# Performance work log

Hardware: AMD Instinct MI355X
Metric: run time of the kernel (lower is better)

## Reference

```python
import jax, jax.numpy as jnp
import numpy as np

B, T, I, H = 64, 2048, 64, 256


def setup_inputs() -> dict:
    key = jax.random.key(0)
    ks = jax.random.split(key, 7)
    s_ih = 1.0 / np.sqrt(H)
    return {
        "x": jax.random.normal(ks[0], (B, T, I), dtype=jnp.float32),
        "W_ih": jax.random.normal(ks[1], (H, I), dtype=jnp.float32) * s_ih,
        "W_hh": jax.random.normal(ks[2], (H, H), dtype=jnp.float32) * s_ih,
        "b_ih": jax.random.normal(ks[3], (H,), dtype=jnp.float32) * s_ih,
        "b_hh": jax.random.normal(ks[4], (H,), dtype=jnp.float32) * s_ih,
        "W_fc": jax.random.normal(ks[5], (1, H), dtype=jnp.float32) * s_ih,
        "b_fc": jax.random.normal(ks[6], (1,), dtype=jnp.float32) * s_ih,
    }


def reference(x, W_ih, W_hh, b_ih, b_hh, W_fc, b_fc):
    # Precompute input projection for all timesteps: [B,T,H]
    pre = jnp.einsum('bti,hi->bth', x, W_ih) + b_ih + b_hh
    pre_t = jnp.swapaxes(pre, 0, 1)  # [T,B,H]

    def step(h, p_t):
        h_new = jnp.tanh(p_t + h @ W_hh.T)
        return h_new, h_new

    h0 = jnp.zeros((x.shape[0], W_hh.shape[0]), dtype=x.dtype)
    _, hs = jax.lax.scan(step, h0, pre_t)  # hs: [T,B,H]
    out = jnp.swapaxes(hs, 0, 1)  # [B,T,H]
    return out @ W_fc.T + b_fc  # [B,T,1]
```

## Files before the change

### kernel.cpp

```cpp
#include <hip/hip_runtime.h>

#define BB 64
#define TT 2048
#define II 64
#define HH 256

typedef __fp16 h2_t __attribute__((ext_vector_type(2)));
typedef __fp16 h8_t __attribute__((ext_vector_type(8)));

#define H2(i) __builtin_bit_cast(h2_t, (i))
#define I32(h) __builtin_bit_cast(int, (h))

#if __has_builtin(__builtin_amdgcn_fdot2)
#define FDOT2(a, b, c) __builtin_amdgcn_fdot2((a), (b), (c), false)
#else
__device__ __forceinline__ float FDOT2(h2_t a, h2_t b, float c) {
    return fmaf((float)a[0], (float)b[0], fmaf((float)a[1], (float)b[1], c));
}
#endif

__device__ __forceinline__ float ftanh(float x) {
    float e = __expf(2.0f * x);
    return 1.0f - 2.0f * __builtin_amdgcn_rcpf(e + 1.0f);
}

template <int CTRL>
__device__ __forceinline__ float dpp_add(float v) {
    int s = __builtin_amdgcn_update_dpp(0, __float_as_int(v), CTRL, 0xF, 0xF, true);
    return v + __int_as_float(s);
}
template <int CTRL>
__device__ __forceinline__ float dpp_get(float v) {
    int s = __builtin_amdgcn_update_dpp(0, __float_as_int(v), CTRL, 0xF, 0xF, true);
    return __int_as_float(s);
}
template <int PAT>
__device__ __forceinline__ float swz_get(float v) {
    return __int_as_float(__builtin_amdgcn_ds_swizzle(__float_as_int(v), PAT));
}
template <int PAT>
__device__ __forceinline__ float swz_add(float v) { return v + swz_get<PAT>(v); }

__device__ __forceinline__ float mrg4(float a, float b, int lane) {
    float t = (lane & 4) ? b : a;
    float u = (lane & 4) ? a : b;
    return t + swz_get<0x101F>(u);
}
__device__ __forceinline__ float mrg2(float a, float b, int lane) {
    float t = (lane & 2) ? b : a;
    float u = (lane & 2) ? a : b;
    return t + dpp_get<0x4E>(u);
}
__device__ __forceinline__ float mrg1(float a, float b, int lane) {
    float t = (lane & 1) ? b : a;
    float u = (lane & 1) ? a : b;
    return t + dpp_get<0xB1>(u);
}

__launch_bounds__(256, 1)
__global__ void rnn_fused(const float* __restrict__ x,
                          const float* __restrict__ W_ih,
                          const float* __restrict__ W_hh,
                          const float* __restrict__ b_ih,
                          const float* __restrict__ b_hh,
                          const float* __restrict__ W_fc,
                          const float* __restrict__ b_fc,
                          float* __restrict__ out) {
    __shared__ __align__(16) __fp16 hbuf[2][320];
    __shared__ float part[TT][8];

    const int tid  = threadIdx.x;
    const int b    = blockIdx.x;
    const int lane = tid & 63;
    const int w    = tid >> 6;
    const int o    = lane >> 3;
    const int q    = lane & 7;

    int whh_i[8][16];
    int wih_i[8][4];
#pragma unroll
    for (int r = 0; r < 8; ++r) {
        const int t_r = w * 64 + o * 8 + r;
        const float4* wr = (const float4*)(W_hh + t_r * HH + q * 32);
#pragma unroll
        for (int jv = 0; jv < 8; ++jv) {
            const float4 wv = wr[jv];
            whh_i[r][jv * 2 + 0] = I32(__builtin_amdgcn_cvt_pkrtz(wv.x, wv.y));
            whh_i[r][jv * 2 + 1] = I32(__builtin_amdgcn_cvt_pkrtz(wv.z, wv.w));
        }
        const float4* wi = (const float4*)(W_ih + t_r * II + q * 8);
        const float4 wa = wi[0], wb = wi[1];
        wih_i[r][0] = I32(__builtin_amdgcn_cvt_pkrtz(wa.x, wa.y));
        wih_i[r][1] = I32(__builtin_amdgcn_cvt_pkrtz(wa.z, wa.w));
        wih_i[r][2] = I32(__builtin_amdgcn_cvt_pkrtz(wb.x, wb.y));
        wih_i[r][3] = I32(__builtin_amdgcn_cvt_pkrtz(wb.z, wb.w));
    }
#pragma unroll
    for (int j = 0; j < 128; ++j) asm volatile("" : "+v"(((int*)whh_i)[j]));
#pragma unroll
    for (int j = 0; j < 32; ++j) asm volatile("" : "+v"(((int*)wih_i)[j]));

    const int myrow = w * 64 + lane;
    const float bias = b_ih[myrow] + b_hh[myrow];
    const float wfc  = W_fc[myrow];
    const float bfc  = b_fc[0];

    for (int idx = tid; idx < 2 * 320; idx += 256) ((__fp16*)hbuf)[idx] = (__fp16)0.0f;
    __syncthreads();

    const float* xbase = x + (size_t)b * TT * II + q * 8;
    float* outb = out + (size_t)b * TT;

    const int hoff = (w * 2 + (lane >> 5)) * 80 + (lane & 31) * 2;
    __fp16* hw0 = (__fp16*)((char*)&hbuf[0][0] + hoff);
    __fp16* hw1 = (__fp16*)((char*)&hbuf[1][0] + hoff);

    h2_t xc[4];
    {
        const float4* xp = (const float4*)(xbase);
        const float4 a = xp[0], c = xp[1];
        xc[0] = __builtin_amdgcn_cvt_pkrtz(a.x, a.y);
        xc[1] = __builtin_amdgcn_cvt_pkrtz(a.z, a.w);
        xc[2] = __builtin_amdgcn_cvt_pkrtz(c.x, c.y);
        xc[3] = __builtin_amdgcn_cvt_pkrtz(c.z, c.w);
    }

    int p = 0;
    for (int i = 0; i < TT; ++i) {
        const int rown = (i + 1 < TT) ? (i + 1) : (TT - 1);
        const float4* xpn = (const float4*)(xbase + rown * II);
        const float4 xna = xpn[0], xnc = xpn[1];

        float a0 = 0, a1 = 0, a2 = 0, a3 = 0, a4 = 0, a5 = 0, a6 = 0, a7 = 0;
        const h8_t* hp = (const h8_t*)((const char*)&hbuf[p][0] + q * 80);
#pragma unroll
        for (int jv = 0; jv < 4; ++jv) {
            const h8_t hv = hp[jv];
#pragma unroll
            for (int e = 0; e < 4; ++e) {
                const h2_t hh2 = __builtin_shufflevector(hv, hv, 0, 1);
                const h2_t he = (e == 0) ? __builtin_shufflevector(hv, hv, 0, 1)
                              : (e == 1) ? __builtin_shufflevector(hv, hv, 2, 3)
                              : (e == 2) ? __builtin_shufflevector(hv, hv, 4, 5)
                                         : __builtin_shufflevector(hv, hv, 6, 7);
                const int j = jv * 4 + e;
                a0 = FDOT2(H2(whh_i[0][j]), he, a0);
                a1 = FDOT2(H2(whh_i[1][j]), he, a1);
                a2 = FDOT2(H2(whh_i[2][j]), he, a2);
                a3 = FDOT2(H2(whh_i[3][j]), he, a3);
                a4 = FDOT2(H2(whh_i[4][j]), he, a4);
                a5 = FDOT2(H2(whh_i[5][j]), he, a5);
                a6 = FDOT2(H2(whh_i[6][j]), he, a6);
                a7 = FDOT2(H2(whh_i[7][j]), he, a7);
                (void)hh2;
            }
        }
#pragma unroll
        for (int e = 0; e < 4; ++e) {
            a0 = FDOT2(H2(wih_i[0][e]), xc[e], a0);
            a1 = FDOT2(H2(wih_i[1][e]), xc[e], a1);
            a2 = FDOT2(H2(wih_i[2][e]), xc[e], a2);
            a3 = FDOT2(H2(wih_i[3][e]), xc[e], a3);
            a4 = FDOT2(H2(wih_i[4][e]), xc[e], a4);
            a5 = FDOT2(H2(wih_i[5][e]), xc[e], a5);
            a6 = FDOT2(H2(wih_i[6][e]), xc[e], a6);
            a7 = FDOT2(H2(wih_i[7][e]), xc[e], a7);
        }

        xc[0] = __builtin_amdgcn_cvt_pkrtz(xna.x, xna.y);
        xc[1] = __builtin_amdgcn_cvt_pkrtz(xna.z, xna.w);
        xc[2] = __builtin_amdgcn_cvt_pkrtz(xnc.x, xnc.y);
        xc[3] = __builtin_amdgcn_cvt_pkrtz(xnc.z, xnc.w);

        const float A0 = mrg4(a0, a4, lane);
        const float A1 = mrg4(a1, a5, lane);
        const float A2 = mrg4(a2, a6, lane);
        const float A3 = mrg4(a3, a7, lane);
        const float B0 = mrg2(A0, A2, lane);
        const float B1 = mrg2(A1, A3, lane);
        const float C0 = mrg1(B0, B1, lane);

        const float hn = ftanh(C0 + bias);
        const int pn = p ^ 1;
        if (pn) hw1[0] = (__fp16)hn; else hw0[0] = (__fp16)hn;

        float c = hn * wfc;
        c = dpp_add<0xB1>(c);
        c = dpp_add<0x4E>(c);
        c = swz_add<0x101F>(c);
        c = dpp_add<0x140>(c);
        c = swz_add<0x401F>(c);
        if ((lane & 31) == 0) part[i][w * 2 + (lane >> 5)] = c;

        __syncthreads();
        p = pn;
    }

    for (int i = tid; i < TT; i += 256) {
        const float4* pp = (const float4*)&part[i][0];
        const float4 s0 = pp[0], s1 = pp[1];
        outb[i] = s0.x + s0.y + s0.z + s0.w + s1.x + s1.y + s1.z + s1.w + bfc;
    }
}

extern "C" void kernel_launch(void* const* d_in, const int* in_sizes, int n_in,
                              void* d_out, int out_size, void* d_ws, size_t ws_size,
                              hipStream_t stream) {
    const float* x    = (const float*)d_in[0];
    const float* W_ih = (const float*)d_in[1];
    const float* W_hh = (const float*)d_in[2];
    const float* b_ih = (const float*)d_in[3];
    const float* b_hh = (const float*)d_in[4];
    const float* W_fc = (const float*)d_in[5];
    const float* b_fc = (const float*)d_in[6];
    float* out = (float*)d_out;

    rnn_fused<<<BB, 256, 0, stream>>>(x, W_ih, W_hh, b_ih, b_hh, W_fc, b_fc, out);
}
```

Measured before the change: 1.323 ms.

## Split recurrent rows across 512 threads with paired lanes per row

Doubles the block to 512 threads so each thread holds 4 rows of W_hh/W_ih instead of 8. This halves the per-step dot-product chain and register footprint, at the cost of one fewer merge stage and each hidden unit being computed redundantly by a lane pair. Only even lanes write h, and W_fc is halved so the duplicated output reduction sums correctly. The output partials buffer is padded to stride 17, and one swizzle in the FC reduction is replaced by a DPP row_half_mirror. The trade-off is more waves taking part in every per-step barrier.

Result: slower. 1.367 ms (+3.4%).

```diff
diff --git a/kernel.cpp b/kernel.cpp
--- a/kernel.cpp
+++ b/kernel.cpp
@@ -4,6 +4,7 @@
 #define TT 2048
 #define II 64
 #define HH 256
+#define PSTR 17
 
 typedef __fp16 h2_t __attribute__((ext_vector_type(2)));
 typedef __fp16 h8_t __attribute__((ext_vector_type(8)));
@@ -51,13 +52,8 @@
     float u = (lane & 2) ? a : b;
     return t + dpp_get<0x4E>(u);
 }
-__device__ __forceinline__ float mrg1(float a, float b, int lane) {
-    float t = (lane & 1) ? b : a;
-    float u = (lane & 1) ? a : b;
-    return t + dpp_get<0xB1>(u);
-}
-
-__launch_bounds__(256, 1)
+
+__launch_bounds__(512, 2)
 __global__ void rnn_fused(const float* __restrict__ x,
                           const float* __restrict__ W_ih,
                           const float* __restrict__ W_hh,
@@ -67,7 +63,7 @@
                           const float* __restrict__ b_fc,
                           float* __restrict__ out) {
     __shared__ __align__(16) __fp16 hbuf[2][320];
-    __shared__ float part[TT][8];
+    __shared__ float part[TT * PSTR];
 
     const int tid  = threadIdx.x;
     const int b    = blockIdx.x;
@@ -76,11 +72,11 @@
     const int o    = lane >> 3;
     const int q    = lane & 7;
 
-    int whh_i[8][16];
-    int wih_i[8][4];
-#pragma unroll
-    for (int r = 0; r < 8; ++r) {
-        const int t_r = w * 64 + o * 8 + r;
+    int whh_i[4][16];
+    int wih_i[4][4];
+#pragma unroll
+    for (int r = 0; r < 4; ++r) {
+        const int t_r = w * 32 + o * 4 + r;
         const float4* wr = (const float4*)(W_hh + t_r * HH + q * 32);
 #pragma unroll
         for (int jv = 0; jv < 8; ++jv) {
@@ -96,22 +92,22 @@
         wih_i[r][3] = I32(__builtin_amdgcn_cvt_pkrtz(wb.z, wb.w));
     }
 #pragma unroll
-    for (int j = 0; j < 128; ++j) asm volatile("" : "+v"(((int*)whh_i)[j]));
-#pragma unroll
-    for (int j = 0; j < 32; ++j) asm volatile("" : "+v"(((int*)wih_i)[j]));
-
-    const int myrow = w * 64 + lane;
+    for (int j = 0; j < 64; ++j) asm volatile("" : "+v"(((int*)whh_i)[j]));
+#pragma unroll
+    for (int j = 0; j < 16; ++j) asm volatile("" : "+v"(((int*)wih_i)[j]));
+
+    const int myrow = w * 32 + o * 4 + ((lane >> 1) & 3);
     const float bias = b_ih[myrow] + b_hh[myrow];
-    const float wfc  = W_fc[myrow];
+    const float wfc  = W_fc[myrow] * 0.5f;
     const float bfc  = b_fc[0];
 
-    for (int idx = tid; idx < 2 * 320; idx += 256) ((__fp16*)hbuf)[idx] = (__fp16)0.0f;
+    for (int idx = tid; idx < 2 * 320; idx += 512) ((__fp16*)hbuf)[idx] = (__fp16)0.0f;
     __syncthreads();
 
     const float* xbase = x + (size_t)b * TT * II + q * 8;
     float* outb = out + (size_t)b * TT;
 
-    const int hoff = (w * 2 + (lane >> 5)) * 80 + (lane & 31) * 2;
+    const int hoff = (myrow >> 5) * 80 + (myrow & 31) * 2;
     __fp16* hw0 = (__fp16*)((char*)&hbuf[0][0] + hoff);
     __fp16* hw1 = (__fp16*)((char*)&hbuf[1][0] + hoff);
 
@@ -131,14 +127,13 @@
         const float4* xpn = (const float4*)(xbase + rown * II);
         const float4 xna = xpn[0], xnc = xpn[1];
 
-        float a0 = 0, a1 = 0, a2 = 0, a3 = 0, a4 = 0, a5 = 0, a6 = 0, a7 = 0;
+        float a0 = 0, a1 = 0, a2 = 0, a3 = 0;
         const h8_t* hp = (const h8_t*)((const char*)&hbuf[p][0] + q * 80);
 #pragma unroll
         for (int jv = 0; jv < 4; ++jv) {
             const h8_t hv = hp[jv];
 #pragma unroll
             for (int e = 0; e < 4; ++e) {
-                const h2_t hh2 = __builtin_shufflevector(hv, hv, 0, 1);
                 const h2_t he = (e == 0) ? __builtin_shufflevector(hv, hv, 0, 1)
                               : (e == 1) ? __builtin_shufflevector(hv, hv, 2, 3)
                               : (e == 2) ? __builtin_shufflevector(hv, hv, 4, 5)
@@ -148,11 +143,6 @@
                 a1 = FDOT2(H2(whh_i[1][j]), he, a1);
                 a2 = FDOT2(H2(whh_i[2][j]), he, a2);
                 a3 = FDOT2(H2(whh_i[3][j]), he, a3);
-                a4 = FDOT2(H2(whh_i[4][j]), he, a4);
-                a5 = FDOT2(H2(whh_i[5][j]), he, a5);
-                a6 = FDOT2(H2(whh_i[6][j]), he, a6);
-                a7 = FDOT2(H2(whh_i[7][j]), he, a7);
-                (void)hh2;
             }
         }
 #pragma unroll
@@ -161,10 +151,6 @@
             a1 = FDOT2(H2(wih_i[1][e]), xc[e], a1);
             a2 = FDOT2(H2(wih_i[2][e]), xc[e], a2);
             a3 = FDOT2(H2(wih_i[3][e]), xc[e], a3);
-            a4 = FDOT2(H2(wih_i[4][e]), xc[e], a4);
-            a5 = FDOT2(H2(wih_i[5][e]), xc[e], a5);
-            a6 = FDOT2(H2(wih_i[6][e]), xc[e], a6);
-            a7 = FDOT2(H2(wih_i[7][e]), xc[e], a7);
         }
 
         xc[0] = __builtin_amdgcn_cvt_pkrtz(xna.x, xna.y);
@@ -172,34 +158,33 @@
         xc[2] = __builtin_amdgcn_cvt_pkrtz(xnc.x, xnc.y);
         xc[3] = __builtin_amdgcn_cvt_pkrtz(xnc.z, xnc.w);
 
-        const float A0 = mrg4(a0, a4, lane);
-        const float A1 = mrg4(a1, a5, lane);
-        const float A2 = mrg4(a2, a6, lane);
-        const float A3 = mrg4(a3, a7, lane);
-        const float B0 = mrg2(A0, A2, lane);
-        const float B1 = mrg2(A1, A3, lane);
-        const float C0 = mrg1(B0, B1, lane);
+        const float A0 = mrg4(a0, a2, lane);
+        const float A1 = mrg4(a1, a3, lane);
+        const float B0 = mrg2(A0, A1, lane);
+        const float C0 = dpp_add<0xB1>(B0);
 
         const float hn = ftanh(C0 + bias);
         const int pn = p ^ 1;
-        if (pn) hw1[0] = (__fp16)hn; else hw0[0] = (__fp16)hn;
+        if (!(lane & 1)) { if (pn) hw1[0] = (__fp16)hn; else hw0[0] = (__fp16)hn; }
 
         float c = hn * wfc;
         c = dpp_add<0xB1>(c);
         c = dpp_add<0x4E>(c);
-        c = swz_add<0x101F>(c);
+        c = dpp_add<0x141>(c);
         c = dpp_add<0x140>(c);
         c = swz_add<0x401F>(c);
-        if ((lane & 31) == 0) part[i][w * 2 + (lane >> 5)] = c;
+        if ((lane & 31) == 0) part[i * PSTR + w * 2 + (lane >> 5)] = c;
 
         __syncthreads();
         p = pn;
     }
 
-    for (int i = tid; i < TT; i += 256) {
-        const float4* pp = (const float4*)&part[i][0];
-        const float4 s0 = pp[0], s1 = pp[1];
-        outb[i] = s0.x + s0.y + s0.z + s0.w + s1.x + s1.y + s1.z + s1.w + bfc;
+    for (int i = tid; i < TT; i += 512) {
+        const float* pp = &part[i * PSTR];
+        float s = bfc;
+#pragma unroll
+        for (int k = 0; k < 16; ++k) s += pp[k];
+        outb[i] = s;
     }
 }
 
@@ -215,5 +200,5 @@
     const float* b_fc = (const float*)d_in[6];
     float* out = (float*)d_out;
 
-    rnn_fused<<<BB, 256, 0, stream>>>(x, W_ih, W_hh, b_ih, b_hh, W_fc, b_fc, out);
-}
+    rnn_fused<<<BB, 512, 0, stream>>>(x, W_ih, W_hh, b_ih, b_hh, W_fc, b_fc, out);
+}
```
